# Optimization experiments

Measured on AMD Instinct MI355X. Metric: run time of the kernel, lower is better.

The kernel has to match this reference:

```python
import jax, jax.numpy as jnp
import numpy as np

AVG_FRAMES_PER_PHONE = 8.0


def setup_inputs() -> dict:
    key = jax.random.key(0)
    k1, k2, k3 = jax.random.split(key, 3)
    B, K, D, T = 16, 512, 256, 4096
    # positive durations averaging ~8 frames per phoneme
    durations = jax.random.uniform(k1, (B, K), dtype=jnp.float32) * (2.0 * AVG_FRAMES_PER_PHONE)
    phoneme = jax.random.normal(k2, (B, D, K), dtype=jnp.float32)
    frame = jax.random.normal(k3, (B, D, T), dtype=jnp.float32)
    return {"durations": durations, "phoneme": phoneme, "frame": frame}


def reference(durations, phoneme, frame):
    """Learnable duration upsampler (NaturalSpeech-style soft alignment).

    durations: (B, K) float frames per phoneme
    phoneme:   (B, D, K)
    frame:     (B, D, T)
    """
    T = frame.shape[-1]
    acc = jnp.cumsum(durations, axis=-1)                 # (B, K) end boundaries
    centers = acc - 0.5 * durations                      # (B, K) phoneme centers
    t = jnp.arange(T, dtype=durations.dtype) + 0.5       # (T,) frame centers
    # energy: negative squared distance frame-center -> phoneme-center
    energy = -((t[None, :, None] - centers[:, None, :]) ** 2)   # (B, T, K)
    w = jax.nn.softmax(energy, axis=-1)                  # soft alignment (B, T, K)
    upsampled = jnp.einsum("btk,bdk->bdt", w, phoneme)   # (B, D, T)
    return upsampled + frame
```

## Files before the change

kernel.cpp:

```cpp
#include <hip/hip_runtime.h>
#include <hip/hip_bf16.h>

#define BK 512
#define BD 256
#define BT 4096
#define W  20
#define DSPLIT 16
#define ROWS (BD / DSPLIT)
#define SROWS 8
#define NSTAGE (ROWS / SROWS)
#define TSPAN 512

typedef __attribute__((address_space(1))) const float gfloat;
typedef __attribute__((address_space(3))) float lfloat;
typedef float v2f __attribute__((ext_vector_type(2)));

__global__ __launch_bounds__(256, 4)
void upsampler_kernel(const float* __restrict__ durations,
                      const float* __restrict__ phoneme,
                      const float* __restrict__ frame,
                      float* __restrict__ out)
{
    const int b   = blockIdx.x;
    const int tt  = blockIdx.y;
    const int ds  = blockIdx.z;
    const int tid = threadIdx.x;

    __shared__ float s_c[BK];
    __shared__ float s_ph[SROWS * BK];
    __shared__ float s_wsum[4];

    const float d0v = durations[b * BK + 2 * tid];
    const float d1v = durations[b * BK + 2 * tid + 1];
    float scan = d0v + d1v;
    #pragma unroll
    for (int off = 1; off < 64; off <<= 1) {
        float other = __shfl_up(scan, off, 64);
        if ((tid & 63) >= off) scan += other;
    }
    if ((tid & 63) == 63) s_wsum[tid >> 6] = scan;
    __syncthreads();
    float woff = 0.f;
    const int wv = tid >> 6;
    for (int i = 0; i < wv; ++i) woff += s_wsum[i];
    const float acc1 = woff + scan;
    s_c[2 * tid]     = (acc1 - d1v) - 0.5f * d0v;
    s_c[2 * tid + 1] = acc1 - 0.5f * d1v;
    __syncthreads();

    const int   t0  = tt * TSPAN + 2 * tid;
    const float tc0 = (float)t0 + 0.5f;
    const float tc1 = (float)t0 + 1.5f;
    const float tcm = (float)t0 + 1.0f;

    int pos = 0;
    #pragma unroll
    for (int st = 256; st > 0; st >>= 1) {
        int np = pos + st;
        if (np <= BK && s_c[np - 1] < tcm) pos = np;
    }
    int wstart = (pos - 10) & ~3;
    wstart = max(0, min(BK - W, wstart));

    float e0[W], e1[W];
    float m0 = -1e30f, m1 = -1e30f;
    #pragma unroll
    for (int j = 0; j < W; ++j) {
        const float c = s_c[wstart + j];
        float a = tc0 - c; e0[j] = -a * a; m0 = fmaxf(m0, e0[j]);
        float bb = tc1 - c; e1[j] = -bb * bb; m1 = fmaxf(m1, e1[j]);
    }
    float s0 = 0.f, s1 = 0.f;
    #pragma unroll
    for (int j = 0; j < W; ++j) {
        e0[j] = __expf(e0[j] - m0); s0 += e0[j];
        e1[j] = __expf(e1[j] - m1); s1 += e1[j];
    }
    const float inv0 = 1.0f / s0, inv1 = 1.0f / s1;
    v2f E0[W / 2], E1[W / 2];
    #pragma unroll
    for (int j = 0; j < W / 2; ++j) {
        E0[j] = (v2f){e0[2 * j] * inv0, e0[2 * j + 1] * inv0};
        E1[j] = (v2f){e1[2 * j] * inv1, e1[2 * j + 1] * inv1};
    }

    const int dlo = ds * ROWS;
    const float* phb  = phoneme + ((size_t)b * BD + dlo) * BK;
    const float* frb  = frame   + ((size_t)b * BD + dlo) * BT + (size_t)tt * TSPAN + 2 * tid;
    float*       outb = out     + ((size_t)b * BD + dlo) * BT + (size_t)tt * TSPAN + 2 * tid;

    for (int sg = 0; sg < NSTAGE; ++sg) {
        float2 fr[SROWS];
        #pragma unroll
        for (int r = 0; r < SROWS; ++r)
            fr[r] = *(const float2*)(frb + (size_t)(sg * SROWS + r) * BT);

        __syncthreads();
        const float* gsrc = phb + (size_t)sg * SROWS * BK;
        #pragma unroll
        for (int c = 0; c < 4; ++c) {
            const int off = (c * 256 + tid) * 4;
            __builtin_amdgcn_global_load_lds((gfloat*)(gsrc + off),
                                             (lfloat*)(s_ph + off), 16, 0, 0);
        }
        asm volatile("s_waitcnt vmcnt(0)" ::: "memory");
        __syncthreads();

        #pragma unroll
        for (int r = 0; r < SROWS; ++r) {
            const float4* sp4 = (const float4*)(s_ph + r * BK + wstart);
            v2f a0 = (v2f){0.f, 0.f}, a1 = (v2f){0.f, 0.f};
            #pragma unroll
            for (int j = 0; j < W / 4; ++j) {
                float4 p = sp4[j];
                v2f lo = (v2f){p.x, p.y};
                v2f hi = (v2f){p.z, p.w};
                a0 = __builtin_elementwise_fma(E0[2 * j],     lo, a0);
                a0 = __builtin_elementwise_fma(E0[2 * j + 1], hi, a0);
                a1 = __builtin_elementwise_fma(E1[2 * j],     lo, a1);
                a1 = __builtin_elementwise_fma(E1[2 * j + 1], hi, a1);
            }
            float2 o;
            o.x = (a0.x + a0.y) + fr[r].x;
            o.y = (a1.x + a1.y) + fr[r].y;
            *(float2*)(outb + (size_t)(sg * SROWS + r) * BT) = o;
        }
    }
}

extern "C" void kernel_launch(void* const* d_in, const int* in_sizes, int n_in,
                              void* d_out, int out_size, void* d_ws, size_t ws_size,
                              hipStream_t stream) {
    const float* durations = (const float*)d_in[0];
    const float* phoneme   = (const float*)d_in[1];
    const float* frame     = (const float*)d_in[2];
    float* out = (float*)d_out;

    dim3 grid(16, BT / TSPAN, DSPLIT);
    upsampler_kernel<<<grid, 256, 0, stream>>>(durations, phoneme, frame, out);
}
```

Before: 129.9 us.

## Compute four frames per thread, double-buffer phoneme LDS tiles, narrow window

Each thread now handles four consecutive frames instead of two, so every float4 phoneme read from LDS feeds four accumulators. TSPAN doubles and the grid shrinks to match. The phoneme stage buffer becomes double-buffered: the next 8-row tile is prefetched via global_load_lds while the current one is consumed. The frame loads widen to float4 and move inside the row loop. The softmax window drops from 20 to 16 phonemes, which cuts exp and FMA work but truncates the alignment more aggressively, and the wider per-thread state raises register pressure.

```diff
diff --git a/kernel.cpp b/kernel.cpp
--- a/kernel.cpp
+++ b/kernel.cpp
@@ -4,12 +4,12 @@
 #define BK 512
 #define BD 256
 #define BT 4096
-#define W  20
+#define W  16
 #define DSPLIT 16
 #define ROWS (BD / DSPLIT)
 #define SROWS 8
 #define NSTAGE (ROWS / SROWS)
-#define TSPAN 512
+#define TSPAN 1024
 
 typedef __attribute__((address_space(1))) const float gfloat;
 typedef __attribute__((address_space(3))) float lfloat;
@@ -27,7 +27,7 @@
     const int tid = threadIdx.x;
 
     __shared__ float s_c[BK];
-    __shared__ float s_ph[SROWS * BK];
+    __shared__ float s_ph[2][SROWS * BK];
     __shared__ float s_wsum[4];
 
     const float d0v = durations[b * BK + 2 * tid];
@@ -48,10 +48,8 @@
     s_c[2 * tid + 1] = acc1 - 0.5f * d1v;
     __syncthreads();
 
-    const int   t0  = tt * TSPAN + 2 * tid;
-    const float tc0 = (float)t0 + 0.5f;
-    const float tc1 = (float)t0 + 1.5f;
-    const float tcm = (float)t0 + 1.0f;
+    const int   t0  = tt * TSPAN + 4 * tid;
+    const float tcm = (float)t0 + 2.0f;
 
     int pos = 0;
     #pragma unroll
@@ -59,71 +57,93 @@
         int np = pos + st;
         if (np <= BK && s_c[np - 1] < tcm) pos = np;
     }
-    int wstart = (pos - 10) & ~3;
+    int wstart = (pos - 8) & ~3;
     wstart = max(0, min(BK - W, wstart));
 
-    float e0[W], e1[W];
-    float m0 = -1e30f, m1 = -1e30f;
+    float e[4][W];
+    float m[4] = {-1e30f, -1e30f, -1e30f, -1e30f};
     #pragma unroll
     for (int j = 0; j < W; ++j) {
         const float c = s_c[wstart + j];
-        float a = tc0 - c; e0[j] = -a * a; m0 = fmaxf(m0, e0[j]);
-        float bb = tc1 - c; e1[j] = -bb * bb; m1 = fmaxf(m1, e1[j]);
+        #pragma unroll
+        for (int o = 0; o < 4; ++o) {
+            float dd = ((float)t0 + 0.5f + (float)o) - c;
+            e[o][j] = -dd * dd;
+            m[o] = fmaxf(m[o], e[o][j]);
+        }
     }
-    float s0 = 0.f, s1 = 0.f;
+    float sum[4] = {0.f, 0.f, 0.f, 0.f};
     #pragma unroll
     for (int j = 0; j < W; ++j) {
-        e0[j] = __expf(e0[j] - m0); s0 += e0[j];
-        e1[j] = __expf(e1[j] - m1); s1 += e1[j];
+        #pragma unroll
+        for (int o = 0; o < 4; ++o) { e[o][j] = __expf(e[o][j] - m[o]); sum[o] += e[o][j]; }
     }
-    const float inv0 = 1.0f / s0, inv1 = 1.0f / s1;
-    v2f E0[W / 2], E1[W / 2];
+    v2f E[4][W / 2];
     #pragma unroll
-    for (int j = 0; j < W / 2; ++j) {
-        E0[j] = (v2f){e0[2 * j] * inv0, e0[2 * j + 1] * inv0};
-        E1[j] = (v2f){e1[2 * j] * inv1, e1[2 * j + 1] * inv1};
+    for (int o = 0; o < 4; ++o) {
+        const float inv = 1.0f / sum[o];
+        #pragma unroll
+        for (int j = 0; j < W / 2; ++j)
+            E[o][j] = (v2f){e[o][2 * j] * inv, e[o][2 * j + 1] * inv};
     }
 
     const int dlo = ds * ROWS;
     const float* phb  = phoneme + ((size_t)b * BD + dlo) * BK;
-    const float* frb  = frame   + ((size_t)b * BD + dlo) * BT + (size_t)tt * TSPAN + 2 * tid;
-    float*       outb = out     + ((size_t)b * BD + dlo) * BT + (size_t)tt * TSPAN + 2 * tid;
+    const float* frb  = frame   + ((size_t)b * BD + dlo) * BT + (size_t)tt * TSPAN + 4 * tid;
+    float*       outb = out     + ((size_t)b * BD + dlo) * BT + (size_t)tt * TSPAN + 4 * tid;
 
-    for (int sg = 0; sg < NSTAGE; ++sg) {
-        float2 fr[SROWS];
-        #pragma unroll
-        for (int r = 0; r < SROWS; ++r)
-            fr[r] = *(const float2*)(frb + (size_t)(sg * SROWS + r) * BT);
-
-        __syncthreads();
-        const float* gsrc = phb + (size_t)sg * SROWS * BK;
+    {
+        const float* gsrc = phb;
         #pragma unroll
         for (int c = 0; c < 4; ++c) {
             const int off = (c * 256 + tid) * 4;
             __builtin_amdgcn_global_load_lds((gfloat*)(gsrc + off),
-                                             (lfloat*)(s_ph + off), 16, 0, 0);
+                                             (lfloat*)(&s_ph[0][0] + off), 16, 0, 0);
         }
+    }
+
+    #pragma unroll
+    for (int sg = 0; sg < NSTAGE; ++sg) {
         asm volatile("s_waitcnt vmcnt(0)" ::: "memory");
         __syncthreads();
 
+        if (sg + 1 < NSTAGE) {
+            const float* gsrc = phb + (size_t)(sg + 1) * SROWS * BK;
+            #pragma unroll
+            for (int c = 0; c < 4; ++c) {
+                const int off = (c * 256 + tid) * 4;
+                __builtin_amdgcn_global_load_lds((gfloat*)(gsrc + off),
+                                                 (lfloat*)(&s_ph[(sg + 1) & 1][0] + off), 16, 0, 0);
+            }
+        }
+
+        const float* bufp = &s_ph[sg & 1][0];
         #pragma unroll
         for (int r = 0; r < SROWS; ++r) {
-            const float4* sp4 = (const float4*)(s_ph + r * BK + wstart);
-            v2f a0 = (v2f){0.f, 0.f}, a1 = (v2f){0.f, 0.f};
+            const int d = sg * SROWS + r;
+            const float4 frv = *(const float4*)(frb + (size_t)d * BT);
+            const float4* sp4 = (const float4*)(bufp + r * BK + wstart);
+            v2f a0 = (v2f){0.f, 0.f}, a1 = a0, a2 = a0, a3 = a0;
             #pragma unroll
-            for (int j = 0; j < W / 4; ++j) {
-                float4 p = sp4[j];
+            for (int q = 0; q < W / 4; ++q) {
+                float4 p = sp4[q];
                 v2f lo = (v2f){p.x, p.y};
                 v2f hi = (v2f){p.z, p.w};
-                a0 = __builtin_elementwise_fma(E0[2 * j],     lo, a0);
-                a0 = __builtin_elementwise_fma(E0[2 * j + 1], hi, a0);
-                a1 = __builtin_elementwise_fma(E1[2 * j],     lo, a1);
-                a1 = __builtin_elementwise_fma(E1[2 * j + 1], hi, a1);
+                a0 = __builtin_elementwise_fma(E[0][2 * q], lo, a0);
+                a0 = __builtin_elementwise_fma(E[0][2 * q + 1], hi, a0);
+                a1 = __builtin_elementwise_fma(E[1][2 * q], lo, a1);
+                a1 = __builtin_elementwise_fma(E[1][2 * q + 1], hi, a1);
+                a2 = __builtin_elementwise_fma(E[2][2 * q], lo, a2);
+                a2 = __builtin_elementwise_fma(E[2][2 * q + 1], hi, a2);
+                a3 = __builtin_elementwise_fma(E[3][2 * q], lo, a3);
+                a3 = __builtin_elementwise_fma(E[3][2 * q + 1], hi, a3);
             }
-            float2 o;
-            o.x = (a0.x + a0.y) + fr[r].x;
-            o.y = (a1.x + a1.y) + fr[r].y;
-            *(float2*)(outb + (size_t)(sg * SROWS + r) * BT) = o;
+            float4 ov;
+            ov.x = (a0.x + a0.y) + frv.x;
+            ov.y = (a1.x + a1.y) + frv.y;
+            ov.z = (a2.x + a2.y) + frv.z;
+            ov.w = (a3.x + a3.y) + frv.w;
+            *(float4*)(outb + (size_t)d * BT) = ov;
         }
     }
 }
```

After: 126.4 us. 1.03x faster.
